# Kernel optimization log

Hardware: AMD Instinct MI355X
Metric: run time of the kernel (lower is better)

## Reference

```python
import jax
import jax.numpy as jnp
import numpy as np

EPS = 1e-06


def _topk_mask(scores, k):
    # scores: (T, E); hard top-k mask along last dim
    _, idx = jax.lax.top_k(scores, k)            # (T, k)
    hard = jax.nn.one_hot(idx, scores.shape[-1]).sum(axis=-2)  # (T, E)
    return hard.astype(bool)


def setup_inputs() -> dict:
    key = jax.random.key(0)
    k1, k2, k3 = jax.random.split(key, 3)
    T, D, E = 8192, 4096, 64
    h_td = jax.random.normal(k1, (T, D), dtype=jnp.float32)
    # eqx.nn.Linear weight layout: (out_features, in_features)
    W = jax.random.normal(k2, (E, D), dtype=jnp.float32) * (1.0 / np.sqrt(D))
    bias_e = jax.random.normal(k3, (E,), dtype=jnp.float32)
    return {"h_td": h_td, "W": W, "bias_e": bias_e, "k": 8}


def reference(h_td, W, bias_e, k):
    # Linear(d_model -> E), no bias in proj; external bias_e added after
    logits_te = jnp.einsum("td,ed->te", h_td, W) + bias_e[None, :]  # (T, E)
    # Soft combine weights always from clean logits
    weight_te = jax.nn.softmax(logits_te, axis=-1)
    # Training path: Gumbel noise on the selection scores only
    gkey = jax.random.key(42)
    u = jax.random.uniform(gkey, logits_te.shape, minval=EPS, maxval=1.0 - EPS)
    g = -jnp.log(-jnp.log(u))
    sel_scores = logits_te + g
    mask_te = _topk_mask(sel_scores, k)
    return (mask_te, weight_te, logits_te)
```

## Files before the change

kernel.cpp:

```cpp
#include <hip/hip_runtime.h>
#include <stdint.h>
#include <math.h>

#define T_DIM 8192
#define D_DIM 4096
#define E_DIM 64
#define TE (T_DIM * E_DIM)
#define GAP_MARGIN 2e-3
#define ROWS 16
#define BK 256
#define NCHUNK (D_DIM / BK)
#define FIX_WAVES 8
#define FIX_COLS (D_DIM / FIX_WAVES)

typedef __attribute__((ext_vector_type(8))) short short8_t;
typedef __attribute__((ext_vector_type(4))) float f32x4;

__device__ __align__(16) short Whi_g[E_DIM * D_DIM];
__device__ __align__(16) short Wlo_g[E_DIM * D_DIM];

__device__ __forceinline__ void threefry2x32_k42(uint32_t x0, uint32_t x1,
                                                 uint32_t& o0, uint32_t& o1) {
  const uint32_t ks0 = 0u, ks1 = 42u;
  const uint32_t ks2 = 0x1BD11BDAu ^ ks0 ^ ks1;
  x0 += ks0; x1 += ks1;
#define TF_RND(r) { x0 += x1; x1 = (x1 << (r)) | (x1 >> (32 - (r))); x1 ^= x0; }
  TF_RND(13) TF_RND(15) TF_RND(26) TF_RND(6)   x0 += ks1; x1 += ks2 + 1u;
  TF_RND(17) TF_RND(29) TF_RND(16) TF_RND(24)  x0 += ks2; x1 += ks0 + 2u;
  TF_RND(13) TF_RND(15) TF_RND(26) TF_RND(6)   x0 += ks0; x1 += ks1 + 3u;
  TF_RND(17) TF_RND(29) TF_RND(16) TF_RND(24)  x0 += ks1; x1 += ks2 + 4u;
  TF_RND(13) TF_RND(15) TF_RND(26) TF_RND(6)   x0 += ks2; x1 += ks0 + 5u;
#undef TF_RND
  o0 = x0; o1 = x1;
}

__device__ __forceinline__ uint32_t jax_random_bits32(uint32_t j) {
  uint32_t o0, o1;
  threefry2x32_k42(0u, j, o0, o1);
  return o0 ^ o1;
}

__device__ __forceinline__ void finalize_row_f64(double logit, int e, int t,
                                                 float& mask_out, float& weight_out,
                                                 double& gap_out) {
  double m = logit;
#pragma unroll
  for (int off = 1; off < 64; off <<= 1) {
    const double om = __shfl_xor(m, off, 64);
    m = (om > m) ? om : m;
  }
  const double pe = exp(logit - m);
  double s = pe;
#pragma unroll
  for (int off = 1; off < 64; off <<= 1) s += __shfl_xor(s, off, 64);
  weight_out = (float)(pe / s);

  const int idx = t * 64 + e;
  const uint32_t bits = jax_random_bits32((uint32_t)idx);
  const float f01 = __uint_as_float((bits >> 9) | 0x3f800000u) - 1.0f;
  const float minv = 1e-6f;
  const float maxv = 0.999999f;
  float u = __fadd_rn(__fmul_rn(f01, maxv - minv), minv);
  u = fmaxf(minv, u);
  const double g = -log(-log((double)u));
  const double sel = logit + g;

  float mask = 0.0f;
  double cur = sel;
  double v8 = 0.0, v9 = 0.0;
  for (int it = 0; it < 9; ++it) {
    double v = cur;
    int vi = e;
#pragma unroll
    for (int off = 1; off < 64; off <<= 1) {
      const double ov = __shfl_xor(v, off, 64);
      const int    oi = __shfl_xor(vi, off, 64);
      if (ov > v || (ov == v && oi < vi)) { v = ov; vi = oi; }
    }
    if (it < 8) {
      if (vi == e) { mask = 1.0f; cur = -__builtin_inf(); }
      if (it == 7) v8 = v;
    } else {
      v9 = v;
    }
  }
  mask_out = mask;
  gap_out = v8 - v9;
}

__device__ __forceinline__ uint16_t f2bf(float f) {
  const uint32_t x = __float_as_uint(f);
  return (uint16_t)((x + 0x7FFFu + ((x >> 16) & 1u)) >> 16);
}

__device__ __forceinline__ void split8(const float4 a, const float4 b,
                                       short8_t& hi, short8_t& lo) {
  const float f[8] = {a.x, a.y, a.z, a.w, b.x, b.y, b.z, b.w};
#pragma unroll
  for (int j = 0; j < 8; ++j) {
    const uint16_t hb = f2bf(f[j]);
    const float fh = __uint_as_float((uint32_t)hb << 16);
    const uint16_t lb = f2bf(f[j] - fh);
    hi[j] = (short)hb;
    lo[j] = (short)lb;
  }
}

__global__ __launch_bounds__(256)
void w_split_kernel(const float* __restrict__ W) {
  const int g = blockIdx.x * 256 + threadIdx.x;
#pragma unroll
  for (int r = 0; r < 2; ++r) {
    const int u = g * 2 + r;
    const int e = u >> 9;
    const int k0 = (u & 511) * 8;
    const float* wp = W + (size_t)e * D_DIM + k0;
    const float4 a = *reinterpret_cast<const float4*>(wp);
    const float4 b = *reinterpret_cast<const float4*>(wp + 4);
    short8_t hi, lo;
    split8(a, b, hi, lo);
    const int ks = k0 >> 5, q = (k0 >> 3) & 3;
    const int subE = e >> 4, ee = e & 15;
    const int idx = ks * 2048 + subE * 512 + q * 128 + ee * 8;
    *reinterpret_cast<short8_t*>(Whi_g + idx) = hi;
    *reinterpret_cast<short8_t*>(Wlo_g + idx) = lo;
  }
}

__global__ __launch_bounds__(256)
void router_mfma_kernel(const float* __restrict__ h,
                        const float* __restrict__ bias,
                        float* __restrict__ out,
                        unsigned char* __restrict__ flags) {
  __shared__ __align__(16) short Ahi[2][ROWS * BK];
  __shared__ __align__(16) short Alo[2][ROWS * BK];
  __shared__ float logits_lds[ROWS * 65];

  const int tid  = threadIdx.x;
  const int wave = tid >> 6;
  const int lane = tid & 63;
  const int row0 = blockIdx.x * ROWS;

  const int r  = tid >> 4;
  const int k0 = (tid & 15) * 16;
  const int sA  = k0 >> 5;
  const int qA  = (k0 >> 3) & 3;
  const int u0A = sA * 64 + qA * 16 + r;
  const int u0B = u0A + 16;
  const int uA  = u0A ^ ((u0A >> 4) & 7);
  const int uB  = u0B ^ ((u0B >> 4) & 7);
  const float* hst = h + (size_t)(row0 + r) * D_DIM + k0;

  const int b_off = wave * 512 + (lane >> 4) * 128 + (lane & 15) * 8;

  f32x4 acc = {0.0f, 0.0f, 0.0f, 0.0f};

  float4 Ra0, Ra1, Ra2, Ra3, Rb0, Rb1, Rb2, Rb3;
  Ra0 = *reinterpret_cast<const float4*>(hst + 0);
  Ra1 = *reinterpret_cast<const float4*>(hst + 4);
  Ra2 = *reinterpret_cast<const float4*>(hst + 8);
  Ra3 = *reinterpret_cast<const float4*>(hst + 12);
  Rb0 = *reinterpret_cast<const float4*>(hst + BK + 0);
  Rb1 = *reinterpret_cast<const float4*>(hst + BK + 4);
  Rb2 = *reinterpret_cast<const float4*>(hst + BK + 8);
  Rb3 = *reinterpret_cast<const float4*>(hst + BK + 12);

#define CHUNK_STEP(R0, R1, R2, R3, BUF, CC)                                    \
  {                                                                            \
    short8_t hi_, lo_;                                                         \
    split8(R0, R1, hi_, lo_);                                                  \
    *reinterpret_cast<short8_t*>(&Ahi[BUF][uA * 8]) = hi_;                     \
    *reinterpret_cast<short8_t*>(&Alo[BUF][uA * 8]) = lo_;                     \
    split8(R2, R3, hi_, lo_);                                                  \
    *reinterpret_cast<short8_t*>(&Ahi[BUF][uB * 8]) = hi_;                     \
    *reinterpret_cast<short8_t*>(&Alo[BUF][uB * 8]) = lo_;                     \
    __syncthreads();                                                           \
    if ((CC) + 2 < NCHUNK) {                                                   \
      const float* p_ = hst + ((CC) + 2) * BK;                                 \
      R0 = *reinterpret_cast<const float4*>(p_ + 0);                           \
      R1 = *reinterpret_cast<const float4*>(p_ + 4);                           \
      R2 = *reinterpret_cast<const float4*>(p_ + 8);                           \
      R3 = *reinterpret_cast<const float4*>(p_ + 12);                          \
    }                                                                          \
    _Pragma("unroll")                                                          \
    for (int s_ = 0; s_ < BK / 32; ++s_) {                                     \
      const int ur0_ = s_ * 64 + lane;                                         \
      const int ur_  = ur0_ ^ ((ur0_ >> 4) & 7);                               \
      const short8_t ah_ = *reinterpret_cast<const short8_t*>(&Ahi[BUF][ur_ * 8]); \
      const short8_t al_ = *reinterpret_cast<const short8_t*>(&Alo[BUF][ur_ * 8]); \
      const size_t bo_ = (size_t)((CC) * (BK / 32) + s_) * 2048 + b_off;       \
      const short8_t bh_ = *reinterpret_cast<const short8_t*>(Whi_g + bo_);    \
      const short8_t bl_ = *reinterpret_cast<const short8_t*>(Wlo_g + bo_);    \
      acc = __builtin_amdgcn_mfma_f32_16x16x32_bf16(al_, bh_, acc, 0, 0, 0);   \
      acc = __builtin_amdgcn_mfma_f32_16x16x32_bf16(ah_, bl_, acc, 0, 0, 0);   \
      acc = __builtin_amdgcn_mfma_f32_16x16x32_bf16(ah_, bh_, acc, 0, 0, 0);   \
    }                                                                          \
  }

  for (int c = 0; c < NCHUNK; c += 2) {
    CHUNK_STEP(Ra0, Ra1, Ra2, Ra3, 0, c)
    CHUNK_STEP(Rb0, Rb1, Rb2, Rb3, 1, c + 1)
  }
#undef CHUNK_STEP

  {
    const int q   = lane >> 4;
    const int col = wave * 16 + (lane & 15);
#pragma unroll
    for (int reg = 0; reg < 4; ++reg) {
      const int m = q * 4 + reg;
      logits_lds[m * 65 + col] = acc[reg];
    }
  }
  __syncthreads();

  const int e = lane;
  const double be = (double)bias[e];
  for (int rr = 0; rr < 4; ++rr) {
    const int rloc = wave * 4 + rr;
    const int t = row0 + rloc;
    const double logit = (double)logits_lds[rloc * 65 + e] + be;

    float mask, weight;
    double gap;
    finalize_row_f64(logit, e, t, mask, weight, gap);

    const int idx = t * 64 + e;
    out[idx]          = mask;
    out[TE + idx]     = weight;
    out[2 * TE + idx] = (float)logit;
    if (e == 0) flags[t] = (gap < GAP_MARGIN) ? 1 : 0;
  }
}

__global__ __launch_bounds__(512)
void router_fixup_kernel(const float* __restrict__ h,
                         const float* __restrict__ W,
                         const float* __restrict__ bias,
                         const unsigned char* __restrict__ flags,
                         float* __restrict__ out) {
  const int t = blockIdx.x;
  if (flags[t] == 0) return;

  __shared__ float  h_lds[D_DIM];
  __shared__ double red[FIX_WAVES][64];

  const int tid  = threadIdx.x;
  const int wv   = tid >> 6;
  const int lane = tid & 63;

  {
    const float4* hrow4 = reinterpret_cast<const float4*>(h + (size_t)t * D_DIM);
    float4* hl4 = reinterpret_cast<float4*>(h_lds);
    hl4[tid]       = hrow4[tid];
    hl4[tid + 512] = hrow4[tid + 512];
  }
  __syncthreads();

  const int e = lane;
  const float* wrow = W + (size_t)e * D_DIM + wv * FIX_COLS;
  const float* hseg = h_lds + wv * FIX_COLS;

  double acc0 = 0.0, acc1 = 0.0, acc2 = 0.0, acc3 = 0.0;
#pragma unroll 8
  for (int c = 0; c < FIX_COLS; c += 16) {
    const float4 w0 = *reinterpret_cast<const float4*>(wrow + c);
    const float4 w1 = *reinterpret_cast<const float4*>(wrow + c + 4);
    const float4 w2 = *reinterpret_cast<const float4*>(wrow + c + 8);
    const float4 w3 = *reinterpret_cast<const float4*>(wrow + c + 12);
    acc0 = fma((double)w0.x, (double)hseg[c + 0], acc0);
    acc0 = fma((double)w0.y, (double)hseg[c + 1], acc0);
    acc0 = fma((double)w0.z, (double)hseg[c + 2], acc0);
    acc0 = fma((double)w0.w, (double)hseg[c + 3], acc0);
    acc1 = fma((double)w1.x, (double)hseg[c + 4], acc1);
    acc1 = fma((double)w1.y, (double)hseg[c + 5], acc1);
    acc1 = fma((double)w1.z, (double)hseg[c + 6], acc1);
    acc1 = fma((double)w1.w, (double)hseg[c + 7], acc1);
    acc2 = fma((double)w2.x, (double)hseg[c + 8], acc2);
    acc2 = fma((double)w2.y, (double)hseg[c + 9], acc2);
    acc2 = fma((double)w2.z, (double)hseg[c + 10], acc2);
    acc2 = fma((double)w2.w, (double)hseg[c + 11], acc2);
    acc3 = fma((double)w3.x, (double)hseg[c + 12], acc3);
    acc3 = fma((double)w3.y, (double)hseg[c + 13], acc3);
    acc3 = fma((double)w3.z, (double)hseg[c + 14], acc3);
    acc3 = fma((double)w3.w, (double)hseg[c + 15], acc3);
  }
  red[wv][e] = (acc0 + acc1) + (acc2 + acc3);
  __syncthreads();

  if (wv == 0) {
    double s = red[0][e];
#pragma unroll
    for (int i = 1; i < FIX_WAVES; ++i) s += red[i][e];
    const double logit = s + (double)bias[e];

    float mask, weight;
    double gap;
    finalize_row_f64(logit, e, t, mask, weight, gap);

    const int idx = t * 64 + e;
    out[idx]          = mask;
    out[TE + idx]     = weight;
    out[2 * TE + idx] = (float)logit;
  }
}

extern "C" void kernel_launch(void* const* d_in, const int* in_sizes, int n_in,
                              void* d_out, int out_size, void* d_ws, size_t ws_size,
                              hipStream_t stream) {
  const float* h    = (const float*)d_in[0];
  const float* W    = (const float*)d_in[1];
  const float* bias = (const float*)d_in[2];
  float* out = (float*)d_out;
  unsigned char* flags = (unsigned char*)d_ws;

  w_split_kernel<<<64, 256, 0, stream>>>(W);
  router_mfma_kernel<<<T_DIM / ROWS, 256, 0, stream>>>(h, bias, out, flags);
  router_fixup_kernel<<<T_DIM, 512, 0, stream>>>(h, W, bias, flags, out);
}
```

Before: 330.6 us.

## Double row tile to 32 with 8 waves, batch W fragment loads per chunk

The MFMA router kernel now handles 32 rows per block using 512 threads arranged as a 2x4 wave grid. Each W fragment is reused by two row tiles, which halves the W traffic per row. All 16 B fragments for a chunk are loaded up front, before the LDS store and barrier, so global latency overlaps the split and sync. The fixup kernel moves to 1024 threads with 16 waves. This raises register and LDS pressure and leaves fewer blocks in the grid.

```diff
diff --git a/kernel.cpp b/kernel.cpp
--- a/kernel.cpp
+++ b/kernel.cpp
@@ -7,14 +7,20 @@
 #define E_DIM 64
 #define TE (T_DIM * E_DIM)
 #define GAP_MARGIN 2e-3
-#define ROWS 16
+#define ROWS 32
 #define BK 256
 #define NCHUNK (D_DIM / BK)
-#define FIX_WAVES 8
+#define FIX_WAVES 16
 #define FIX_COLS (D_DIM / FIX_WAVES)
 
 typedef __attribute__((ext_vector_type(8))) short short8_t;
 typedef __attribute__((ext_vector_type(4))) float f32x4;
+
+#define BAR() do {                                            \
+    asm volatile("s_waitcnt lgkmcnt(0)" ::: "memory");        \
+    __builtin_amdgcn_s_barrier();                             \
+    asm volatile("" ::: "memory");                            \
+  } while (0)
 
 __device__ __align__(16) short Whi_g[E_DIM * D_DIM];
 __device__ __align__(16) short Wlo_g[E_DIM * D_DIM];
@@ -127,7 +133,7 @@
   }
 }
 
-__global__ __launch_bounds__(256)
+__global__ __launch_bounds__(512, 2)
 void router_mfma_kernel(const float* __restrict__ h,
                         const float* __restrict__ bias,
                         float* __restrict__ out,
@@ -139,19 +145,23 @@
   const int tid  = threadIdx.x;
   const int wave = tid >> 6;
   const int lane = tid & 63;
+  const int m    = wave >> 2;
+  const int n    = wave & 3;
   const int row0 = blockIdx.x * ROWS;
 
   const int r  = tid >> 4;
   const int k0 = (tid & 15) * 16;
-  const int sA  = k0 >> 5;
-  const int qA  = (k0 >> 3) & 3;
-  const int u0A = sA * 64 + qA * 16 + r;
-  const int u0B = u0A + 16;
-  const int uA  = u0A ^ ((u0A >> 4) & 7);
-  const int uB  = u0B ^ ((u0B >> 4) & 7);
+  const int sW  = (tid & 15) >> 1;
+  const int qW  = ((tid & 15) & 1) * 2;
+  const int u0A = sW * 128 + qW * 32 + r;
+  const int u0B = u0A + 32;
+  const int uA  = u0A ^ ((u0A >> 5) & 7);
+  const int uB  = u0B ^ ((u0B >> 5) & 7);
   const float* hst = h + (size_t)(row0 + r) * D_DIM + k0;
 
-  const int b_off = wave * 512 + (lane >> 4) * 128 + (lane & 15) * 8;
+  const int ar0 = (lane >> 4) * 32 + m * 16 + (lane & 15);
+
+  const int b_off = n * 512 + (lane >> 4) * 128 + (lane & 15) * 8;
 
   f32x4 acc = {0.0f, 0.0f, 0.0f, 0.0f};
 
@@ -165,16 +175,48 @@
   Rb2 = *reinterpret_cast<const float4*>(hst + BK + 8);
   Rb3 = *reinterpret_cast<const float4*>(hst + BK + 12);
 
+#define KSTEP(S, BH, BL)                                                       \
+  {                                                                            \
+    const int ur0_ = (S) * 128 + ar0;                                          \
+    const int ur_  = ur0_ ^ ((ur0_ >> 5) & 7);                                 \
+    const short8_t ah_ = *reinterpret_cast<const short8_t*>(&Ahi[BUF_][ur_ * 8]); \
+    const short8_t al_ = *reinterpret_cast<const short8_t*>(&Alo[BUF_][ur_ * 8]); \
+    acc = __builtin_amdgcn_mfma_f32_16x16x32_bf16(al_, BH, acc, 0, 0, 0);      \
+    acc = __builtin_amdgcn_mfma_f32_16x16x32_bf16(ah_, BL, acc, 0, 0, 0);      \
+    acc = __builtin_amdgcn_mfma_f32_16x16x32_bf16(ah_, BH, acc, 0, 0, 0);      \
+  }
+
 #define CHUNK_STEP(R0, R1, R2, R3, BUF, CC)                                    \
   {                                                                            \
+    const int BUF_ = (BUF);                                                    \
+               \
+    const size_t bb_ = (size_t)((CC) * 8) * 2048 + b_off;                      \
+    const short8_t BH0 = *reinterpret_cast<const short8_t*>(Whi_g + bb_ + 0 * 2048); \
+    const short8_t BH1 = *reinterpret_cast<const short8_t*>(Whi_g + bb_ + 1 * 2048); \
+    const short8_t BH2 = *reinterpret_cast<const short8_t*>(Whi_g + bb_ + 2 * 2048); \
+    const short8_t BH3 = *reinterpret_cast<const short8_t*>(Whi_g + bb_ + 3 * 2048); \
+    const short8_t BH4 = *reinterpret_cast<const short8_t*>(Whi_g + bb_ + 4 * 2048); \
+    const short8_t BH5 = *reinterpret_cast<const short8_t*>(Whi_g + bb_ + 5 * 2048); \
+    const short8_t BH6 = *reinterpret_cast<const short8_t*>(Whi_g + bb_ + 6 * 2048); \
+    const short8_t BH7 = *reinterpret_cast<const short8_t*>(Whi_g + bb_ + 7 * 2048); \
+    const short8_t BL0 = *reinterpret_cast<const short8_t*>(Wlo_g + bb_ + 0 * 2048); \
+    const short8_t BL1 = *reinterpret_cast<const short8_t*>(Wlo_g + bb_ + 1 * 2048); \
+    const short8_t BL2 = *reinterpret_cast<const short8_t*>(Wlo_g + bb_ + 2 * 2048); \
+    const short8_t BL3 = *reinterpret_cast<const short8_t*>(Wlo_g + bb_ + 3 * 2048); \
+    const short8_t BL4 = *reinterpret_cast<const short8_t*>(Wlo_g + bb_ + 4 * 2048); \
+    const short8_t BL5 = *reinterpret_cast<const short8_t*>(Wlo_g + bb_ + 5 * 2048); \
+    const short8_t BL6 = *reinterpret_cast<const short8_t*>(Wlo_g + bb_ + 6 * 2048); \
+    const short8_t BL7 = *reinterpret_cast<const short8_t*>(Wlo_g + bb_ + 7 * 2048); \
+          \
     short8_t hi_, lo_;                                                         \
     split8(R0, R1, hi_, lo_);                                                  \
-    *reinterpret_cast<short8_t*>(&Ahi[BUF][uA * 8]) = hi_;                     \
-    *reinterpret_cast<short8_t*>(&Alo[BUF][uA * 8]) = lo_;                     \
+    *reinterpret_cast<short8_t*>(&Ahi[BUF_][uA * 8]) = hi_;                    \
+    *reinterpret_cast<short8_t*>(&Alo[BUF_][uA * 8]) = lo_;                    \
     split8(R2, R3, hi_, lo_);                                                  \
-    *reinterpret_cast<short8_t*>(&Ahi[BUF][uB * 8]) = hi_;                     \
-    *reinterpret_cast<short8_t*>(&Alo[BUF][uB * 8]) = lo_;                     \
-    __syncthreads();                                                           \
+    *reinterpret_cast<short8_t*>(&Ahi[BUF_][uB * 8]) = hi_;                    \
+    *reinterpret_cast<short8_t*>(&Alo[BUF_][uB * 8]) = lo_;                    \
+    BAR();                                                                     \
+                \
     if ((CC) + 2 < NCHUNK) {                                                   \
       const float* p_ = hst + ((CC) + 2) * BK;                                 \
       R0 = *reinterpret_cast<const float4*>(p_ + 0);                           \
@@ -182,19 +224,9 @@
       R2 = *reinterpret_cast<const float4*>(p_ + 8);                           \
       R3 = *reinterpret_cast<const float4*>(p_ + 12);                          \
     }                                                                          \
-    _Pragma("unroll")                                                          \
-    for (int s_ = 0; s_ < BK / 32; ++s_) {                                     \
-      const int ur0_ = s_ * 64 + lane;                                         \
-      const int ur_  = ur0_ ^ ((ur0_ >> 4) & 7);                               \
-      const short8_t ah_ = *reinterpret_cast<const short8_t*>(&Ahi[BUF][ur_ * 8]); \
-      const short8_t al_ = *reinterpret_cast<const short8_t*>(&Alo[BUF][ur_ * 8]); \
-      const size_t bo_ = (size_t)((CC) * (BK / 32) + s_) * 2048 + b_off;       \
-      const short8_t bh_ = *reinterpret_cast<const short8_t*>(Whi_g + bo_);    \
-      const short8_t bl_ = *reinterpret_cast<const short8_t*>(Wlo_g + bo_);    \
-      acc = __builtin_amdgcn_mfma_f32_16x16x32_bf16(al_, bh_, acc, 0, 0, 0);   \
-      acc = __builtin_amdgcn_mfma_f32_16x16x32_bf16(ah_, bl_, acc, 0, 0, 0);   \
-      acc = __builtin_amdgcn_mfma_f32_16x16x32_bf16(ah_, bh_, acc, 0, 0, 0);   \
-    }                                                                          \
+    KSTEP(0, BH0, BL0) KSTEP(1, BH1, BL1) KSTEP(2, BH2, BL2)                   \
+    KSTEP(3, BH3, BL3) KSTEP(4, BH4, BL4) KSTEP(5, BH5, BL5)                   \
+    KSTEP(6, BH6, BL6) KSTEP(7, BH7, BL7)                                      \
   }
 
   for (int c = 0; c < NCHUNK; c += 2) {
@@ -202,14 +234,15 @@
     CHUNK_STEP(Rb0, Rb1, Rb2, Rb3, 1, c + 1)
   }
 #undef CHUNK_STEP
+#undef KSTEP
 
   {
     const int q   = lane >> 4;
-    const int col = wave * 16 + (lane & 15);
+    const int col = n * 16 + (lane & 15);
 #pragma unroll
     for (int reg = 0; reg < 4; ++reg) {
-      const int m = q * 4 + reg;
-      logits_lds[m * 65 + col] = acc[reg];
+      const int mr = m * 16 + q * 4 + reg;
+      logits_lds[mr * 65 + col] = acc[reg];
     }
   }
   __syncthreads();
@@ -233,7 +266,7 @@
   }
 }
 
-__global__ __launch_bounds__(512)
+__global__ __launch_bounds__(1024)
 void router_fixup_kernel(const float* __restrict__ h,
                          const float* __restrict__ W,
                          const float* __restrict__ bias,
@@ -251,9 +284,7 @@
 
   {
     const float4* hrow4 = reinterpret_cast<const float4*>(h + (size_t)t * D_DIM);
-    float4* hl4 = reinterpret_cast<float4*>(h_lds);
-    hl4[tid]       = hrow4[tid];
-    hl4[tid + 512] = hrow4[tid + 512];
+    reinterpret_cast<float4*>(h_lds)[tid] = hrow4[tid];
   }
   __syncthreads();
 
@@ -262,7 +293,7 @@
   const float* hseg = h_lds + wv * FIX_COLS;
 
   double acc0 = 0.0, acc1 = 0.0, acc2 = 0.0, acc3 = 0.0;
-#pragma unroll 8
+#pragma unroll 4
   for (int c = 0; c < FIX_COLS; c += 16) {
     const float4 w0 = *reinterpret_cast<const float4*>(wrow + c);
     const float4 w1 = *reinterpret_cast<const float4*>(wrow + c + 4);
@@ -315,6 +346,6 @@
   unsigned char* flags = (unsigned char*)d_ws;
 
   w_split_kernel<<<64, 256, 0, stream>>>(W);
-  router_mfma_kernel<<<T_DIM / ROWS, 256, 0, stream>>>(h, bias, out, flags);
-  router_fixup_kernel<<<T_DIM, 512, 0, stream>>>(h, W, bias, flags, out);
-}
+  router_mfma_kernel<<<T_DIM / ROWS, 512, 0, stream>>>(h, bias, out, flags);
+  router_fixup_kernel<<<T_DIM, 1024, 0, stream>>>(h, W, bias, flags, out);
+}
```

Result: faster. 305.7 us (-7.6%).
